# Kernel optimization log

Hardware: AMD Instinct MI355X
Metric: run time of the kernel (lower is better)

## Reference

```python
import jax, jax.numpy as jnp
import numpy as np

N_NODES = 100000
N_EDGES = 1600000
IN_FEATS, N_HIDDEN, N_CLASSES = 128, 64, 40


def setup_inputs() -> dict:
    key = jax.random.key(0)
    ks = jax.random.split(key, 6)
    h = jax.random.normal(ks[0], (N_NODES, IN_FEATS), dtype=jnp.float32)
    W0 = jax.random.normal(ks[1], (IN_FEATS, N_HIDDEN), dtype=jnp.float32) * (1.0 / np.sqrt(IN_FEATS))
    b0 = jnp.zeros((N_HIDDEN,), dtype=jnp.float32)
    W1 = jax.random.normal(ks[2], (N_HIDDEN, N_HIDDEN), dtype=jnp.float32) * (1.0 / np.sqrt(N_HIDDEN))
    b1 = jnp.zeros((N_HIDDEN,), dtype=jnp.float32)
    W2 = jax.random.normal(ks[3], (N_HIDDEN, N_CLASSES), dtype=jnp.float32) * (1.0 / np.sqrt(N_HIDDEN))
    b2 = jnp.zeros((N_CLASSES,), dtype=jnp.float32)
    src = jax.random.randint(ks[4], (N_EDGES,), 0, N_NODES, dtype=jnp.int32)
    dst = jax.random.randint(ks[5], (N_EDGES,), 0, N_NODES, dtype=jnp.int32)
    return {"h": h, "W0": W0, "b0": b0, "W1": W1, "b1": b1, "W2": W2, "b2": b2, "src": src, "dst": dst}


def _degrees(src, dst):
    ones = jnp.ones(src.shape[0], dtype=jnp.float32)
    out_deg = jax.ops.segment_sum(ones, src, num_segments=N_NODES)
    in_deg = jax.ops.segment_sum(ones, dst, num_segments=N_NODES)
    # DGL clamps degrees to >= 1 (allow_zero_in_degree)
    norm_src = jax.lax.rsqrt(jnp.maximum(out_deg, 1.0))  # [N]
    norm_dst = jax.lax.rsqrt(jnp.maximum(in_deg, 1.0))   # [N]
    return norm_src, norm_dst


def _graph_conv(x, W, b, src, dst, norm_src, norm_dst, act):
    # DGL GraphConv, norm='both': D_in^{-1/2} A^T D_out^{-1/2} (X W) + b
    xw = (x @ W) * norm_src[:, None]               # [N, out]
    agg = jax.ops.segment_sum(xw[src], dst, num_segments=N_NODES)  # gather-scatter over edges
    out = agg * norm_dst[:, None] + b
    return jax.nn.relu(out) if act else out


def reference(h, W0, b0, W1, b1, W2, b2, src, dst):
    norm_src, norm_dst = _degrees(src, dst)
    h = _graph_conv(h, W0, b0, src, dst, norm_src, norm_dst, act=True)
    # dropout layers are identity at inference
    h = _graph_conv(h, W1, b1, src, dst, norm_src, norm_dst, act=True)
    h = _graph_conv(h, W2, b2, src, dst, norm_src, norm_dst, act=False)
    return h
```

## Files before the change

kernel.cpp:

```cpp
#include <hip/hip_runtime.h>
#include <hip/hip_fp16.h>

#define N_NODES 100000
#define N_EDGES 1600000
#define ELL_W 64
#define NCHUNK 32
#define NSEG 8
#define CH (N_EDGES / NCHUNK)
#define SEGN (N_NODES / NSEG)

typedef _Float16 half8 __attribute__((ext_vector_type(8)));
typedef float floatx4 __attribute__((ext_vector_type(4)));


__global__ __launch_bounds__(512) void k_count(const int* __restrict__ src, const int* __restrict__ dst,
                                               unsigned char* __restrict__ cnt_out,
                                               unsigned char* __restrict__ cnt_in) {
    __shared__ int ci[SEGN];
    __shared__ int co[SEGN];
    const int c = blockIdx.x;
    const int lo = blockIdx.y * SEGN;
    for (int i = threadIdx.x; i < SEGN; i += 512) { ci[i] = 0; co[i] = 0; }
    __syncthreads();
    const int4* s4 = (const int4*)(src + c * CH);
    const int4* d4 = (const int4*)(dst + c * CH);
    for (int i = threadIdx.x; i < CH / 4; i += 512) {
        int4 s = s4[i], d = d4[i];
        unsigned a;
        a = (unsigned)(s.x - lo); if (a < SEGN) atomicAdd(&co[a], 1);
        a = (unsigned)(s.y - lo); if (a < SEGN) atomicAdd(&co[a], 1);
        a = (unsigned)(s.z - lo); if (a < SEGN) atomicAdd(&co[a], 1);
        a = (unsigned)(s.w - lo); if (a < SEGN) atomicAdd(&co[a], 1);
        a = (unsigned)(d.x - lo); if (a < SEGN) atomicAdd(&ci[a], 1);
        a = (unsigned)(d.y - lo); if (a < SEGN) atomicAdd(&ci[a], 1);
        a = (unsigned)(d.z - lo); if (a < SEGN) atomicAdd(&ci[a], 1);
        a = (unsigned)(d.w - lo); if (a < SEGN) atomicAdd(&ci[a], 1);
    }
    __syncthreads();
    for (int i = threadIdx.x; i < SEGN; i += 512) {
        cnt_in [c * N_NODES + lo + i] = (unsigned char)ci[i];
        cnt_out[c * N_NODES + lo + i] = (unsigned char)co[i];
    }
}

__global__ __launch_bounds__(256) void k_scan(unsigned char* __restrict__ cnt_in,
                                              const unsigned char* __restrict__ cnt_out,
                                              int* __restrict__ fill, float* __restrict__ norm_src,
                                              float* __restrict__ norm_dst) {
    int d = blockIdx.x * 256 + threadIdx.x;
    if (d >= N_NODES) return;
    int run = 0;
    #pragma unroll
    for (int c = 0; c < NCHUNK; ++c) {
        int v = cnt_in[c * N_NODES + d];
        cnt_in[c * N_NODES + d] = (unsigned char)run;
        run += v;
    }
    int od = 0;
    #pragma unroll
    for (int c = 0; c < NCHUNK; ++c) od += cnt_out[c * N_NODES + d];
    fill[d] = run;
    norm_dst[d] = rsqrtf((float)(run < 1 ? 1 : run));
    norm_src[d] = rsqrtf((float)(od  < 1 ? 1 : od ));
}

__global__ __launch_bounds__(512) void k_scatter(const int* __restrict__ src, const int* __restrict__ dst,
                                                 const unsigned char* __restrict__ bases,
                                                 int* __restrict__ ell) {
    __shared__ int base[SEGN];
    const int c = blockIdx.x;
    const int lo = blockIdx.y * SEGN;
    for (int i = threadIdx.x; i < SEGN; i += 512) base[i] = bases[c * N_NODES + lo + i];
    __syncthreads();
    const int4* s4 = (const int4*)(src + c * CH);
    const int4* d4 = (const int4*)(dst + c * CH);
    for (int i = threadIdx.x; i < CH / 4; i += 512) {
        int4 s = s4[i], d = d4[i];
        unsigned r; int p;
        r = (unsigned)(d.x - lo); if (r < SEGN) { p = atomicAdd(&base[r], 1); if (p < ELL_W) ell[p * N_NODES + lo + r] = s.x; }
        r = (unsigned)(d.y - lo); if (r < SEGN) { p = atomicAdd(&base[r], 1); if (p < ELL_W) ell[p * N_NODES + lo + r] = s.y; }
        r = (unsigned)(d.z - lo); if (r < SEGN) { p = atomicAdd(&base[r], 1); if (p < ELL_W) ell[p * N_NODES + lo + r] = s.z; }
        r = (unsigned)(d.w - lo); if (r < SEGN) { p = atomicAdd(&base[r], 1); if (p < ELL_W) ell[p * N_NODES + lo + r] = s.w; }
    }
}

template<int K, int NCOL>
__global__ __launch_bounds__(256) void k_gemm(const float* __restrict__ Xv, const float* __restrict__ W,
                                              const float* __restrict__ norm, __half* __restrict__ Y) {
    constexpr int NT = (NCOL + 15) / 16;
    constexpr int NR = NT * 16;
    __shared__ __align__(16) _Float16 Xh[64][K + 8];
    __shared__ __align__(16) _Float16 Wt[NR][K + 8];
    const int tid = threadIdx.x;
    const int row0 = blockIdx.x * 64;

    for (int idx = tid; idx < K * NCOL; idx += 256) {
        int k = idx / NCOL, c = idx - (idx / NCOL) * NCOL;
        Wt[c][k] = (_Float16)W[idx];
    }
    for (int idx = tid; idx < (NR - NCOL) * K; idx += 256) {
        int c = NCOL + idx / K, k = idx - (idx / K) * K;
        Wt[c][k] = (_Float16)0;
    }

    for (int idx = tid; idx < 64 * (K / 8); idx += 256) {
        int r = idx / (K / 8), kc = idx - (idx / (K / 8)) * (K / 8);
        int gr = row0 + r;
        half8 v = {0, 0, 0, 0, 0, 0, 0, 0};
        if (gr < N_NODES) {
            const float* X = Xv + (long)gr * K + kc * 8;
            float4 u0 = *(const float4*)(X + 0);
            float4 u1 = *(const float4*)(X + 4);
            v.s0 = (_Float16)u0.x; v.s1 = (_Float16)u0.y;
            v.s2 = (_Float16)u0.z; v.s3 = (_Float16)u0.w;
            v.s4 = (_Float16)u1.x; v.s5 = (_Float16)u1.y;
            v.s6 = (_Float16)u1.z; v.s7 = (_Float16)u1.w;
        }
        *(half8*)&Xh[r][kc * 8] = v;
    }
    __syncthreads();

    const int lane = tid & 63;
    const int wave = tid >> 6;
    const int quad = lane >> 4;
    const int l16 = lane & 15;
    const int r0 = wave * 16;

    floatx4 acc[NT] = {};
    #pragma unroll
    for (int k0 = 0; k0 < K; k0 += 32) {
        half8 a = *(const half8*)&Xh[r0 + l16][k0 + quad * 8];
        #pragma unroll
        for (int t = 0; t < NT; ++t) {
            half8 b = *(const half8*)&Wt[t * 16 + l16][k0 + quad * 8];
            acc[t] = __builtin_amdgcn_mfma_f32_16x16x32_f16(a, b, acc[t], 0, 0, 0);
        }
    }

    #pragma unroll
    for (int i = 0; i < 4; ++i) {
        int gr = row0 + r0 + quad * 4 + i;
        if (gr < N_NODES) {
            float s = norm[gr];
            #pragma unroll
            for (int t = 0; t < NT; ++t) {
                int c = t * 16 + l16;
                if (c < NCOL) Y[(long)gr * NCOL + c] = __float2half(acc[t][i] * s);
            }
        }
    }
}

template<int K, int NCOL>
__global__ __launch_bounds__(256) void k_agg_gemm(const __half* __restrict__ XWp, const int* __restrict__ ell,
                                                  const int* __restrict__ deg, const float* __restrict__ norm_dst,
                                                  const float* __restrict__ biasp, const float* __restrict__ W,
                                                  const float* __restrict__ norm, __half* __restrict__ Y) {
    constexpr int NT = (NCOL + 15) / 16;
    constexpr int NR = NT * 16;
    constexpr int NQ = K / 8;
    __shared__ __align__(16) _Float16 Xh[64][K + 8];
    __shared__ __align__(16) _Float16 Wt[NR][K + 8];
    __shared__ int sIdx[64][65];
    __shared__ int sDeg[64];
    __shared__ int sMax;
    const int tid = threadIdx.x;
    const int row0 = blockIdx.x * 64;

    for (int idx = tid; idx < K * NCOL; idx += 256) {
        int k = idx / NCOL, c = idx - (idx / NCOL) * NCOL;
        Wt[c][k] = (_Float16)W[idx];
    }
    for (int idx = tid; idx < (NR - NCOL) * K; idx += 256) {
        int c = NCOL + idx / K, k = idx - (idx / K) * K;
        Wt[c][k] = (_Float16)0;
    }

    if (tid < 64) {
        int node = row0 + tid;
        int dg = 0;
        if (node < N_NODES) { dg = deg[node]; if (dg > ELL_W) dg = ELL_W; }
        sDeg[tid] = dg;
        int v = dg;
        #pragma unroll
        for (int o = 32; o > 0; o >>= 1) v = max(v, __shfl_down(v, o));
        if (tid == 0) sMax = v;
    }
    __syncthreads();
    const int mdeg = sMax;
    for (int i = tid; i < mdeg * 64; i += 256) {
        int slot = i >> 6, r = i & 63;
        int node = row0 + r;
        sIdx[r][slot] = (node < N_NODES) ? ell[slot * N_NODES + node] : 0;
    }
    __syncthreads();

    for (int item = tid; item < 64 * NQ; item += 256) {
        int r = item / NQ, q = item - (item / NQ) * NQ;
        int d = row0 + r;
        int dg = sDeg[r];
        const int* idxr = sIdx[r];
        float acc[8] = {};
        int j = 0;
        for (; j + 8 <= dg; j += 8) {
            float4 v[8];
            #pragma unroll
            for (int u = 0; u < 8; ++u)
                v[u] = *(const float4*)(XWp + (long)idxr[j + u] * K + q * 8);
            #pragma unroll
            for (int u = 0; u < 8; ++u) {
                const __half2* hh = (const __half2*)&v[u];
                #pragma unroll
                for (int t = 0; t < 4; ++t) {
                    float2 f = __half22float2(hh[t]);
                    acc[2 * t + 0] += f.x;
                    acc[2 * t + 1] += f.y;
                }
            }
        }
        for (; j < dg; ++j) {
            float4 rv = *(const float4*)(XWp + (long)idxr[j] * K + q * 8);
            const __half2* hh = (const __half2*)&rv;
            #pragma unroll
            for (int t = 0; t < 4; ++t) {
                float2 f = __half22float2(hh[t]);
                acc[2 * t + 0] += f.x;
                acc[2 * t + 1] += f.y;
            }
        }
        _Float16 res[8] = {};
        if (d < N_NODES) {
            float nd = norm_dst[d];
            #pragma unroll
            for (int t = 0; t < 8; ++t) {
                float o = acc[t] * nd + biasp[q * 8 + t];
                res[t] = (_Float16)fmaxf(o, 0.f);
            }
        }
        *(half8*)&Xh[r][q * 8] = *(const half8*)res;
    }
    __syncthreads();

    const int lane = tid & 63;
    const int wave = tid >> 6;
    const int quad = lane >> 4;
    const int l16 = lane & 15;
    const int r0 = wave * 16;

    floatx4 acc[NT] = {};
    #pragma unroll
    for (int k0 = 0; k0 < K; k0 += 32) {
        half8 a = *(const half8*)&Xh[r0 + l16][k0 + quad * 8];
        #pragma unroll
        for (int t = 0; t < NT; ++t) {
            half8 b = *(const half8*)&Wt[t * 16 + l16][k0 + quad * 8];
            acc[t] = __builtin_amdgcn_mfma_f32_16x16x32_f16(a, b, acc[t], 0, 0, 0);
        }
    }

    #pragma unroll
    for (int i = 0; i < 4; ++i) {
        int gr = row0 + r0 + quad * 4 + i;
        if (gr < N_NODES) {
            float s = norm[gr];
            #pragma unroll
            for (int t = 0; t < NT; ++t) {
                int c = t * 16 + l16;
                if (c < NCOL) Y[(long)gr * NCOL + c] = __float2half(acc[t][i] * s);
            }
        }
    }
}

template<int NF>
__global__ __launch_bounds__(320) void k_agg_f(const __half* __restrict__ XW, const int* __restrict__ ell,
                                               const int* __restrict__ deg, const float* __restrict__ norm_dst,
                                               const float* __restrict__ bias, float* __restrict__ OUT) {
    constexpr int NQ = NF / 8;
    __shared__ int sIdx[64][65];
    __shared__ int sDeg[64];
    __shared__ int sMax;
    const int tid = threadIdx.x;
    const int row0 = blockIdx.x * 64;

    if (tid < 64) {
        int node = row0 + tid;
        int dg = 0;
        if (node < N_NODES) { dg = deg[node]; if (dg > ELL_W) dg = ELL_W; }
        sDeg[tid] = dg;
        int v = dg;
        #pragma unroll
        for (int o = 32; o > 0; o >>= 1) v = max(v, __shfl_down(v, o));
        if (tid == 0) sMax = v;
    }
    __syncthreads();
    const int mdeg = sMax;
    for (int i = tid; i < mdeg * 64; i += 320) {
        int slot = i >> 6, r = i & 63;
        int node = row0 + r;
        sIdx[r][slot] = (node < N_NODES) ? ell[slot * N_NODES + node] : 0;
    }
    __syncthreads();

    const int r = tid / NQ, q = tid - (tid / NQ) * NQ;
    const int d = row0 + r;
    if (d >= N_NODES) return;
    const int dg = sDeg[r];
    const int* idxr = sIdx[r];

    float acc[8] = {};
    int j = 0;
    for (; j + 8 <= dg; j += 8) {
        float4 v[8];
        #pragma unroll
        for (int u = 0; u < 8; ++u)
            v[u] = *(const float4*)(XW + (long)idxr[j + u] * NF + q * 8);
        #pragma unroll
        for (int u = 0; u < 8; ++u) {
            const __half2* hh = (const __half2*)&v[u];
            #pragma unroll
            for (int t = 0; t < 4; ++t) {
                float2 f = __half22float2(hh[t]);
                acc[2 * t + 0] += f.x;
                acc[2 * t + 1] += f.y;
            }
        }
    }
    for (; j < dg; ++j) {
        float4 rv = *(const float4*)(XW + (long)idxr[j] * NF + q * 8);
        const __half2* hh = (const __half2*)&rv;
        #pragma unroll
        for (int t = 0; t < 4; ++t) {
            float2 f = __half22float2(hh[t]);
            acc[2 * t + 0] += f.x;
            acc[2 * t + 1] += f.y;
        }
    }

    float nd = norm_dst[d];
    float o[8];
    #pragma unroll
    for (int t = 0; t < 8; ++t) o[t] = acc[t] * nd + bias[q * 8 + t];
    *(float4*)(OUT + (long)d * NF + q * 8 + 0) = make_float4(o[0], o[1], o[2], o[3]);
    *(float4*)(OUT + (long)d * NF + q * 8 + 4) = make_float4(o[4], o[5], o[6], o[7]);
}

extern "C" void kernel_launch(void* const* d_in, const int* in_sizes, int n_in,
                              void* d_out, int out_size, void* d_ws, size_t ws_size,
                              hipStream_t stream) {
    const float* h  = (const float*)d_in[0];
    const float* W0 = (const float*)d_in[1];
    const float* b0 = (const float*)d_in[2];
    const float* W1 = (const float*)d_in[3];
    const float* b1 = (const float*)d_in[4];
    const float* W2 = (const float*)d_in[5];
    const float* b2 = (const float*)d_in[6];
    const int* src  = (const int*)d_in[7];
    const int* dst  = (const int*)d_in[8];
    float* out = (float*)d_out;

    char* ws = (char*)d_ws;
    size_t off = 0;
    int* fill        = (int*)(ws + off); off += (size_t)N_NODES * 4;
    float* norm_src  = (float*)(ws + off); off += (size_t)N_NODES * 4;
    float* norm_dst  = (float*)(ws + off); off += (size_t)N_NODES * 4;
    int* ell         = (int*)(ws + off); off += (size_t)N_NODES * ELL_W * 4;
    unsigned char* cnt_in  = (unsigned char*)(ws + off); off += (size_t)NCHUNK * N_NODES;
    unsigned char* cnt_out = (unsigned char*)(ws + off); off += (size_t)NCHUNK * N_NODES;
    __half* bufA  = (__half*)(ws + off); off += (size_t)N_NODES * 64 * 2;
    __half* bufB  = (__half*)(ws + off); off += (size_t)N_NODES * 64 * 2;

    k_count<<<dim3(NCHUNK, NSEG), 512, 0, stream>>>(src, dst, cnt_out, cnt_in);
    k_scan<<<(N_NODES + 255) / 256, 256, 0, stream>>>(cnt_in, cnt_out, fill, norm_src, norm_dst);
    k_scatter<<<dim3(NCHUNK, NSEG), 512, 0, stream>>>(src, dst, cnt_in, ell);

    const int grid = (N_NODES + 63) / 64;

    k_gemm<128, 64><<<grid, 256, 0, stream>>>(h, W0, norm_src, bufA);
    k_agg_gemm<64, 64><<<grid, 256, 0, stream>>>(bufA, ell, fill, norm_dst, b0, W1, norm_src, bufB);
    k_agg_gemm<64, 40><<<grid, 256, 0, stream>>>(bufB, ell, fill, norm_dst, b1, W2, norm_src, bufA);
    k_agg_f<40><<<grid, 320, 0, stream>>>(bufA, ell, fill, norm_dst, b2, out);
}
```

Before: 275.9 us.

## Pack degree counters into 16-bit LDS halves and double-buffer gather loads

The degree count and ELL scatter kernels now pack two 16-bit counters into each 32-bit shared word. This halves LDS use, which allows fewer node segments (4) and more edge chunks (64), so edges are re-read fewer times. The gather loops in the fused aggregation kernels are double-buffered, so the next 8 neighbor rows load while the current 8 are accumulated. This adds register pressure and relies on per-chunk counts staying below 256 for the byte-wide count arrays.

```diff
diff --git a/kernel.cpp b/kernel.cpp
--- a/kernel.cpp
+++ b/kernel.cpp
@@ -4,8 +4,8 @@
 #define N_NODES 100000
 #define N_EDGES 1600000
 #define ELL_W 64
-#define NCHUNK 32
-#define NSEG 8
+#define NCHUNK 64
+#define NSEG 4
 #define CH (N_EDGES / NCHUNK)
 #define SEGN (N_NODES / NSEG)
 
@@ -16,30 +16,30 @@
 __global__ __launch_bounds__(512) void k_count(const int* __restrict__ src, const int* __restrict__ dst,
                                                unsigned char* __restrict__ cnt_out,
                                                unsigned char* __restrict__ cnt_in) {
-    __shared__ int ci[SEGN];
-    __shared__ int co[SEGN];
+    __shared__ unsigned pk[SEGN];
     const int c = blockIdx.x;
     const int lo = blockIdx.y * SEGN;
-    for (int i = threadIdx.x; i < SEGN; i += 512) { ci[i] = 0; co[i] = 0; }
+    for (int i = threadIdx.x; i < SEGN; i += 512) pk[i] = 0;
     __syncthreads();
     const int4* s4 = (const int4*)(src + c * CH);
     const int4* d4 = (const int4*)(dst + c * CH);
     for (int i = threadIdx.x; i < CH / 4; i += 512) {
         int4 s = s4[i], d = d4[i];
         unsigned a;
-        a = (unsigned)(s.x - lo); if (a < SEGN) atomicAdd(&co[a], 1);
-        a = (unsigned)(s.y - lo); if (a < SEGN) atomicAdd(&co[a], 1);
-        a = (unsigned)(s.z - lo); if (a < SEGN) atomicAdd(&co[a], 1);
-        a = (unsigned)(s.w - lo); if (a < SEGN) atomicAdd(&co[a], 1);
-        a = (unsigned)(d.x - lo); if (a < SEGN) atomicAdd(&ci[a], 1);
-        a = (unsigned)(d.y - lo); if (a < SEGN) atomicAdd(&ci[a], 1);
-        a = (unsigned)(d.z - lo); if (a < SEGN) atomicAdd(&ci[a], 1);
-        a = (unsigned)(d.w - lo); if (a < SEGN) atomicAdd(&ci[a], 1);
+        a = (unsigned)(s.x - lo); if (a < SEGN) atomicAdd(&pk[a], 0x10000u);
+        a = (unsigned)(s.y - lo); if (a < SEGN) atomicAdd(&pk[a], 0x10000u);
+        a = (unsigned)(s.z - lo); if (a < SEGN) atomicAdd(&pk[a], 0x10000u);
+        a = (unsigned)(s.w - lo); if (a < SEGN) atomicAdd(&pk[a], 0x10000u);
+        a = (unsigned)(d.x - lo); if (a < SEGN) atomicAdd(&pk[a], 1u);
+        a = (unsigned)(d.y - lo); if (a < SEGN) atomicAdd(&pk[a], 1u);
+        a = (unsigned)(d.z - lo); if (a < SEGN) atomicAdd(&pk[a], 1u);
+        a = (unsigned)(d.w - lo); if (a < SEGN) atomicAdd(&pk[a], 1u);
     }
     __syncthreads();
     for (int i = threadIdx.x; i < SEGN; i += 512) {
-        cnt_in [c * N_NODES + lo + i] = (unsigned char)ci[i];
-        cnt_out[c * N_NODES + lo + i] = (unsigned char)co[i];
+        unsigned v = pk[i];
+        cnt_in [c * N_NODES + lo + i] = (unsigned char)(v & 0xFFFF);
+        cnt_out[c * N_NODES + lo + i] = (unsigned char)(v >> 16);
     }
 }
 
@@ -50,14 +50,12 @@
     int d = blockIdx.x * 256 + threadIdx.x;
     if (d >= N_NODES) return;
     int run = 0;
-    #pragma unroll
     for (int c = 0; c < NCHUNK; ++c) {
         int v = cnt_in[c * N_NODES + d];
         cnt_in[c * N_NODES + d] = (unsigned char)run;
         run += v;
     }
     int od = 0;
-    #pragma unroll
     for (int c = 0; c < NCHUNK; ++c) od += cnt_out[c * N_NODES + d];
     fill[d] = run;
     norm_dst[d] = rsqrtf((float)(run < 1 ? 1 : run));
@@ -67,20 +65,34 @@
 __global__ __launch_bounds__(512) void k_scatter(const int* __restrict__ src, const int* __restrict__ dst,
                                                  const unsigned char* __restrict__ bases,
                                                  int* __restrict__ ell) {
-    __shared__ int base[SEGN];
+    __shared__ unsigned base[SEGN / 2];
     const int c = blockIdx.x;
     const int lo = blockIdx.y * SEGN;
-    for (int i = threadIdx.x; i < SEGN; i += 512) base[i] = bases[c * N_NODES + lo + i];
+    for (int i = threadIdx.x; i < SEGN / 2; i += 512) {
+        unsigned b0 = bases[c * N_NODES + lo + 2 * i];
+        unsigned b1 = bases[c * N_NODES + lo + 2 * i + 1];
+        base[i] = b0 | (b1 << 16);
+    }
     __syncthreads();
     const int4* s4 = (const int4*)(src + c * CH);
     const int4* d4 = (const int4*)(dst + c * CH);
     for (int i = threadIdx.x; i < CH / 4; i += 512) {
         int4 s = s4[i], d = d4[i];
-        unsigned r; int p;
-        r = (unsigned)(d.x - lo); if (r < SEGN) { p = atomicAdd(&base[r], 1); if (p < ELL_W) ell[p * N_NODES + lo + r] = s.x; }
-        r = (unsigned)(d.y - lo); if (r < SEGN) { p = atomicAdd(&base[r], 1); if (p < ELL_W) ell[p * N_NODES + lo + r] = s.y; }
-        r = (unsigned)(d.z - lo); if (r < SEGN) { p = atomicAdd(&base[r], 1); if (p < ELL_W) ell[p * N_NODES + lo + r] = s.z; }
-        r = (unsigned)(d.w - lo); if (r < SEGN) { p = atomicAdd(&base[r], 1); if (p < ELL_W) ell[p * N_NODES + lo + r] = s.w; }
+        unsigned r, sh, old; int p;
+        r = (unsigned)(d.x - lo); if (r < SEGN) { sh = (r & 1) << 4; old = atomicAdd(&base[r >> 1], 1u << sh); p = (old >> sh) & 0xFFFF; if (p < ELL_W) ell[p * N_NODES + lo + r] = s.x; }
+        r = (unsigned)(d.y - lo); if (r < SEGN) { sh = (r & 1) << 4; old = atomicAdd(&base[r >> 1], 1u << sh); p = (old >> sh) & 0xFFFF; if (p < ELL_W) ell[p * N_NODES + lo + r] = s.y; }
+        r = (unsigned)(d.z - lo); if (r < SEGN) { sh = (r & 1) << 4; old = atomicAdd(&base[r >> 1], 1u << sh); p = (old >> sh) & 0xFFFF; if (p < ELL_W) ell[p * N_NODES + lo + r] = s.z; }
+        r = (unsigned)(d.w - lo); if (r < SEGN) { sh = (r & 1) << 4; old = atomicAdd(&base[r >> 1], 1u << sh); p = (old >> sh) & 0xFFFF; if (p < ELL_W) ell[p * N_NODES + lo + r] = s.w; }
+    }
+}
+
+__device__ __forceinline__ void acc16B(const float4& v, float* acc) {
+    const __half2* hh = (const __half2*)&v;
+    #pragma unroll
+    for (int t = 0; t < 4; ++t) {
+        float2 f = __half22float2(hh[t]);
+        acc[2 * t + 0] += f.x;
+        acc[2 * t + 1] += f.y;
     }
 }
 
@@ -202,31 +214,39 @@
         const int* idxr = sIdx[r];
         float acc[8] = {};
         int j = 0;
-        for (; j + 8 <= dg; j += 8) {
-            float4 v[8];
+        if (dg >= 8) {
+            float4 va[8], vb[8];
             #pragma unroll
-            for (int u = 0; u < 8; ++u)
-                v[u] = *(const float4*)(XWp + (long)idxr[j + u] * K + q * 8);
-            #pragma unroll
-            for (int u = 0; u < 8; ++u) {
-                const __half2* hh = (const __half2*)&v[u];
-                #pragma unroll
-                for (int t = 0; t < 4; ++t) {
-                    float2 f = __half22float2(hh[t]);
-                    acc[2 * t + 0] += f.x;
-                    acc[2 * t + 1] += f.y;
+            for (int u = 0; u < 8; ++u) va[u] = *(const float4*)(XWp + (long)idxr[u] * K + q * 8);
+            j = 8;
+            for (;;) {
+                if (j + 8 <= dg) {
+                    #pragma unroll
+                    for (int u = 0; u < 8; ++u) vb[u] = *(const float4*)(XWp + (long)idxr[j + u] * K + q * 8);
+                    #pragma unroll
+                    for (int u = 0; u < 8; ++u) acc16B(va[u], acc);
+                    j += 8;
+                } else {
+                    #pragma unroll
+                    for (int u = 0; u < 8; ++u) acc16B(va[u], acc);
+                    break;
+                }
+                if (j + 8 <= dg) {
+                    #pragma unroll
+                    for (int u = 0; u < 8; ++u) va[u] = *(const float4*)(XWp + (long)idxr[j + u] * K + q * 8);
+                    #pragma unroll
+                    for (int u = 0; u < 8; ++u) acc16B(vb[u], acc);
+                    j += 8;
+                } else {
+                    #pragma unroll
+                    for (int u = 0; u < 8; ++u) acc16B(vb[u], acc);
+                    break;
                 }
             }
         }
         for (; j < dg; ++j) {
             float4 rv = *(const float4*)(XWp + (long)idxr[j] * K + q * 8);
-            const __half2* hh = (const __half2*)&rv;
-            #pragma unroll
-            for (int t = 0; t < 4; ++t) {
-                float2 f = __half22float2(hh[t]);
-                acc[2 * t + 0] += f.x;
-                acc[2 * t + 1] += f.y;
-            }
+            acc16B(rv, acc);
         }
         _Float16 res[8] = {};
         if (d < N_NODES) {
@@ -310,31 +330,39 @@
 
     float acc[8] = {};
     int j = 0;
-    for (; j + 8 <= dg; j += 8) {
-        float4 v[8];
+    if (dg >= 8) {
+        float4 va[8], vb[8];
         #pragma unroll
-        for (int u = 0; u < 8; ++u)
-            v[u] = *(const float4*)(XW + (long)idxr[j + u] * NF + q * 8);
-        #pragma unroll
-        for (int u = 0; u < 8; ++u) {
-            const __half2* hh = (const __half2*)&v[u];
-            #pragma unroll
-            for (int t = 0; t < 4; ++t) {
-                float2 f = __half22float2(hh[t]);
-                acc[2 * t + 0] += f.x;
-                acc[2 * t + 1] += f.y;
+        for (int u = 0; u < 8; ++u) va[u] = *(const float4*)(XW + (long)idxr[u] * NF + q * 8);
+        j = 8;
+        for (;;) {
+            if (j + 8 <= dg) {
+                #pragma unroll
+                for (int u = 0; u < 8; ++u) vb[u] = *(const float4*)(XW + (long)idxr[j + u] * NF + q * 8);
+                #pragma unroll
+                for (int u = 0; u < 8; ++u) acc16B(va[u], acc);
+                j += 8;
+            } else {
+                #pragma unroll
+                for (int u = 0; u < 8; ++u) acc16B(va[u], acc);
+                break;
+            }
+            if (j + 8 <= dg) {
+                #pragma unroll
+                for (int u = 0; u < 8; ++u) va[u] = *(const float4*)(XW + (long)idxr[j + u] * NF + q * 8);
+                #pragma unroll
+                for (int u = 0; u < 8; ++u) acc16B(vb[u], acc);
+                j += 8;
+            } else {
+                #pragma unroll
+                for (int u = 0; u < 8; ++u) acc16B(vb[u], acc);
+                break;
             }
         }
     }
     for (; j < dg; ++j) {
         float4 rv = *(const float4*)(XW + (long)idxr[j] * NF + q * 8);
-        const __half2* hh = (const __half2*)&rv;
-        #pragma unroll
-        for (int t = 0; t < 4; ++t) {
-            float2 f = __half22float2(hh[t]);
-            acc[2 * t + 0] += f.x;
-            acc[2 * t + 1] += f.y;
-        }
+        acc16B(rv, acc);
     }
 
     float nd = norm_dst[d];
```

Result: slower. 299.9 us (+8.7%).
